# Kernel tuning notes

Measured on AMD Instinct MI355X. Metric: run time of the kernel, lower is better.

## Reference

```python
import jax, jax.numpy as jnp
import numpy as np
from jax import lax


def ternarize(w):
    # TWN-style ternarization: threshold delta = 0.7*mean|w|, scale alpha =
    # mean |w| over surviving entries; straight-through in backward.
    aw = jnp.abs(w)
    delta = 0.7 * jnp.mean(aw)
    mask = (aw > delta).astype(w.dtype)
    alpha = jnp.sum(aw * mask) / jnp.maximum(jnp.sum(mask), 1.0)
    q = alpha * jnp.sign(w) * mask
    return w + lax.stop_gradient(q - w)


def conv2d(x, w, b):
    # x: [N,C,H,W], w: [O,I,kh,kw]
    y = lax.conv_general_dilated(x, w, window_strides=(1, 1), padding='VALID',
                                 dimension_numbers=('NCHW', 'OIHW', 'NCHW'))
    return y + b[None, :, None, None]


def maxpool2(x):
    return lax.reduce_window(x, -jnp.inf, lax.max,
                             window_dimensions=(1, 1, 2, 2),
                             window_strides=(1, 1, 2, 2), padding='VALID')


def setup_inputs() -> dict:
    key = jax.random.key(0)
    ks = jax.random.split(key, 11)
    n_classes = 10
    x = jax.random.normal(ks[0], (1024, 1, 32, 32), dtype=jnp.float32)
    # Kaiming-ish scaled params
    w1 = jax.random.normal(ks[1], (32, 1, 5, 5), jnp.float32) * (1.0 / np.sqrt(1 * 25))
    b1 = jnp.zeros((32,), jnp.float32)
    w2 = jax.random.normal(ks[2], (64, 32, 5, 5), jnp.float32) * (1.0 / np.sqrt(32 * 25))
    b2 = jnp.zeros((64,), jnp.float32)
    w3 = jax.random.normal(ks[3], (120, 64, 5, 5), jnp.float32) * (1.0 / np.sqrt(64 * 25))
    b3 = jnp.zeros((120,), jnp.float32)
    fw1 = jax.random.normal(ks[4], (84, 120), jnp.float32) * (1.0 / np.sqrt(120))
    fb1 = jnp.zeros((84,), jnp.float32)
    fw2 = jax.random.normal(ks[5], (n_classes, 84), jnp.float32) * (1.0 / np.sqrt(84))
    fb2 = jnp.zeros((n_classes,), jnp.float32)
    return {"x": x, "w1": w1, "b1": b1, "w2": w2, "b2": b2,
            "w3": w3, "b3": b3, "fw1": fw1, "fb1": fb1, "fw2": fw2, "fb2": fb2}


def reference(x, w1, b1, w2, b2, w3, b3, fw1, fb1, fw2, fb2):
    h = jnp.tanh(conv2d(x, ternarize(w1), b1))   # [N,32,28,28]
    h = maxpool2(h)                              # [N,32,14,14]
    h = jnp.tanh(conv2d(h, ternarize(w2), b2))   # [N,64,10,10]
    h = maxpool2(h)                              # [N,64,5,5]
    h = jnp.tanh(conv2d(h, ternarize(w3), b3))   # [N,120,1,1]
    h = h.reshape(h.shape[0], -1)                # [N,120]
    h = jnp.tanh(h @ ternarize(fw1).T + fb1)     # [N,84]
    logits = h @ ternarize(fw2).T + fb2          # [N,n_classes]
    probs = jax.nn.softmax(logits, axis=1)
    return (logits, probs)
```

## Files before the change

kernel.cpp:

```cpp
#include <hip/hip_runtime.h>
#include <hip/hip_bf16.h>
#include <math.h>


typedef __attribute__((ext_vector_type(8))) short bf16x8;
typedef __attribute__((ext_vector_type(4))) float f32x4;

static const size_t OFF_PB    = 0;
static const size_t OFF_W1B   = 256;
static const size_t OFF_W2B   = 1056;
static const size_t OFF_W3B   = 26656;
static const size_t OFF_FW1T  = 129056;
static const size_t OFF_FW2T  = 139136;
static const size_t OFF_P2B   = 139976;
static const size_t OFF_H3    = 959176;

#define BPT 16

__device__ __forceinline__ ushort f2bf(float v) {
    unsigned u = __float_as_uint(v);
    unsigned r = (u + 0x7FFFu + ((u >> 16) & 1u)) >> 16;
    return (ushort)r;
}
__device__ __forceinline__ float bf2f(ushort h) {
    return __uint_as_float((unsigned)h << 16);
}

__device__ __forceinline__ float tanh_fast(float x) {
    float e = __expf(-2.0f * fabsf(x));
    float r = 1.0f - 2.0f * e / (1.0f + e);
    return copysignf(r, x);
}

__device__ __forceinline__ void tensor_select(int tensor,
        const float* w1, const float* w2, const float* w3,
        const float* fw1, const float* fw2,
        const float*& src, int& O, int& K) {
    switch (tensor) {
        case 0: src = w1;  O = 32;  K = 25;   break;
        case 1: src = w2;  O = 64;  K = 800;  break;
        case 2: src = w3;  O = 120; K = 1600; break;
        case 3: src = fw1; O = 84;  K = 120;  break;
        default: src = fw2; O = 10; K = 84;   break;
    }
}

__device__ __forceinline__ float block_sum_256(float v, float* sbuf) {
    #pragma unroll
    for (int off = 32; off > 0; off >>= 1) v += __shfl_down(v, off);
    const int wid = threadIdx.x >> 6;
    if ((threadIdx.x & 63) == 0) sbuf[wid] = v;
    __syncthreads();
    return sbuf[0] + sbuf[1] + sbuf[2] + sbuf[3];
}

__device__ __forceinline__ float alpha_of(const float* pb, int tensor) {
    float s1 = 0.f, c = 0.f;
    #pragma unroll
    for (int i = 0; i < BPT; ++i) {
        s1 += pb[80 + tensor * BPT + i];
        c  += pb[160 + tensor * BPT + i];
    }
    return s1 / fmaxf(c, 1.0f);
}

__global__ __launch_bounds__(256)
void tern_pass1(const float* w1, const float* w2, const float* w3,
                const float* fw1, const float* fw2, float* pb) {
    __shared__ float sbuf[4];
    const int tensor = blockIdx.x / BPT;
    const int blk    = blockIdx.x % BPT;
    const float* src; int O, K;
    tensor_select(tensor, w1, w2, w3, fw1, fw2, src, O, K);
    const int n = O * K;
    float s = 0.f;
    for (int i = blk * 256 + threadIdx.x; i < n; i += BPT * 256)
        s += fabsf(src[i]);
    s = block_sum_256(s, sbuf);
    if (threadIdx.x == 0) pb[tensor * BPT + blk] = s;
}

__global__ __launch_bounds__(256)
void tern_pass2(const float* w1, const float* w2, const float* w3,
                const float* fw1, const float* fw2,
                ushort* w1b, ushort* w2b, ushort* w3b,
                float* fw1t, float* fw2t, float* pb) {
    __shared__ float sbuf[4];
    const int tensor = blockIdx.x / BPT;
    const int blk    = blockIdx.x % BPT;
    const float* src; int O, K;
    tensor_select(tensor, w1, w2, w3, fw1, fw2, src, O, K);
    const int n = O * K;
    float tot = 0.f;
    #pragma unroll
    for (int i = 0; i < BPT; ++i) tot += pb[tensor * BPT + i];
    const float delta = 0.7f * tot / (float)n;

    const ushort BP = 0x3F80u, BN = 0xBF80u;
    float s1 = 0.f, cnt = 0.f;

    if (tensor == 0) {
        for (int j = blk * 256 + threadIdx.x; j < 1024; j += BPT * 256) {
            const int oc = j >> 5, kk = j & 31;
            ushort qb = 0;
            if (kk < 25) {
                float w = src[oc * 25 + kk];
                float aw = fabsf(w);
                if (aw > delta) { s1 += aw; cnt += 1.f; qb = (w > 0.f) ? BP : BN; }
            }
            w1b[j] = qb;
        }
    } else if (tensor == 2) {
        for (int i = blk * 256 + threadIdx.x; i < 128 * 1600; i += BPT * 256) {
            ushort qb = 0;
            if (i < n) {
                float w = src[i];
                float aw = fabsf(w);
                if (aw > delta) { s1 += aw; cnt += 1.f; qb = (w > 0.f) ? BP : BN; }
            }
            w3b[i] = qb;
        }
    } else if (tensor == 1) {
        for (int i = blk * 256 + threadIdx.x; i < n; i += BPT * 256) {
            float w = src[i];
            float aw = fabsf(w);
            ushort qb = 0;
            if (aw > delta) { s1 += aw; cnt += 1.f; qb = (w > 0.f) ? BP : BN; }
            int oc = i / 800;
            int r  = i - oc * 800;
            int ic = r / 25;
            int tap = r - ic * 25;
            w2b[oc * 800 + tap * 32 + ic] = qb;
        }
    } else {
        float* dst = (tensor == 3) ? fw1t : fw2t;
        for (int i = blk * 256 + threadIdx.x; i < n; i += BPT * 256) {
            float w = src[i];
            float aw = fabsf(w);
            float q = 0.f;
            if (aw > delta) { s1 += aw; cnt += 1.f; q = (w > 0.f) ? 1.f : -1.f; }
            int o = i / K;
            int k = i - o * K;
            dst[k * O + o] = q;
        }
    }
    s1 = block_sum_256(s1, sbuf);
    __syncthreads();
    cnt = block_sum_256(cnt, sbuf);
    if (threadIdx.x == 0) {
        pb[80 + tensor * BPT + blk]  = s1;
        pb[160 + tensor * BPT + blk] = cnt;
    }
}

#define C2PF 4
__device__ __forceinline__ void conv2_all(
        const ushort* __restrict__ w2b, const ushort* sxt,
        int n0, int mt0, int lane, f32x4 acc[4][2]) {
    const int col = lane & 15, quad = lane >> 4;
    const ushort* abase[4];
    #pragma unroll
    for (int mi = 0; mi < 4; ++mi) {
        int m = (mt0 + mi) * 16 + col;
        m = m < 100 ? m : 99;
        const int oh = m / 10, ow = m - oh * 10;
        abase[mi] = sxt + (oh * 14 + ow) * 40 + quad * 8;
    }
    const ushort* wb0 = w2b + (size_t)(n0 + col) * 800 + quad * 8;
    const ushort* wb1 = wb0 + 16 * 800;
    bf16x8 pb0[C2PF], pb1[C2PF];
    #pragma unroll
    for (int i = 0; i < C2PF; ++i) {
        pb0[i] = *(const bf16x8*)(wb0 + i * 32);
        pb1[i] = *(const bf16x8*)(wb1 + i * 32);
    }
    #pragma unroll
    for (int tap = 0; tap < 25; ++tap) {
        const int slot = tap & (C2PF - 1);
        const bf16x8 b0 = pb0[slot];
        const bf16x8 b1 = pb1[slot];
        if (tap + C2PF < 25) {
            pb0[slot] = *(const bf16x8*)(wb0 + (tap + C2PF) * 32);
            pb1[slot] = *(const bf16x8*)(wb1 + (tap + C2PF) * 32);
        }
        const int kh = tap / 5, kw = tap - kh * 5;
        const int aoff = (kh * 14 + kw) * 40;
        #pragma unroll
        for (int mi = 0; mi < 4; ++mi) {
            bf16x8 af = *(const bf16x8*)(abase[mi] + aoff);
            acc[mi][0] = __builtin_amdgcn_mfma_f32_16x16x32_bf16(af, b0, acc[mi][0], 0, 0, 0);
            acc[mi][1] = __builtin_amdgcn_mfma_f32_16x16x32_bf16(af, b1, acc[mi][1], 0, 0, 0);
        }
    }
}

__global__ __launch_bounds__(256, 4)
void conv12_kernel(const float* __restrict__ x, const ushort* __restrict__ w1b,
                   const float* __restrict__ b1, const ushort* __restrict__ w2b,
                   const float* __restrict__ b2, const float* __restrict__ pb,
                   ushort* __restrict__ p2b) {
    __shared__ __align__(16) char smem[40776];
    ushort* A      = (ushort*)smem;
    ushort* sxt    = (ushort*)smem;
    ushort* hb1    = (ushort*)(smem + 15680);
    float*  hb2    = (float*) (smem + 15680);
    ushort* sxb    = (ushort*)(smem + 38720);
    float*  salpha = (float*) (smem + 40768);

    const int n = blockIdx.x;
    const int t = threadIdx.x;
    const int wave = t >> 6, lane = t & 63;
    const int col = lane & 15, quad = lane >> 4;

    bf16x8 B0 = *(const bf16x8*)(w1b + col * 32 + quad * 8);
    bf16x8 B1 = *(const bf16x8*)(w1b + (col + 16) * 32 + quad * 8);

    {
        float4 v = ((const float4*)(x + (size_t)n * 1024))[t];
        ushort4 q;
        q.x = f2bf(v.x); q.y = f2bf(v.y); q.z = f2bf(v.z); q.w = f2bf(v.w);
        *(ushort4*)(sxb + t * 4) = q;
        if (t == 0) salpha[0] = alpha_of(pb, 0);
        if (t == 1) salpha[1] = alpha_of(pb, 1);
    }
    __syncthreads();

    #pragma unroll
    for (int c = 0; c < 4; ++c) {
        const int tbase = c * 13;
        const int ct    = (c == 3) ? 10 : 13;
        const int pbase = tbase * 16;
        const int rows  = ct * 16;

        for (int r = t; r < rows; r += 256) {
            const int p = pbase + r;
            const int oh = p / 28, ow = p % 28;
            ushort v[25];
            #pragma unroll
            for (int kh = 0; kh < 5; ++kh) {
                const ushort* rr = sxb + (oh + kh) * 32 + ow;
                v[kh*5+0]=rr[0]; v[kh*5+1]=rr[1]; v[kh*5+2]=rr[2];
                v[kh*5+3]=rr[3]; v[kh*5+4]=rr[4];
            }
            uint2* arow = (uint2*)(A + r * 36);
            #pragma unroll
            for (int j = 0; j < 6; ++j) {
                uint2 w;
                w.x = (unsigned)v[4*j]   | ((unsigned)v[4*j+1] << 16);
                w.y = (unsigned)v[4*j+2] | ((unsigned)v[4*j+3] << 16);
                arow[j] = w;
            }
            uint2 w6; w6.x = (unsigned)v[24]; w6.y = 0u;
            arow[6] = w6;
            uint2 w7; w7.x = 0u; w7.y = 0u;
            arow[7] = w7;
        }
        __syncthreads();

        for (int tl = wave; tl < ct; tl += 4) {
            const ushort* ap = A + (tl * 16 + col) * 36 + quad * 8;
            ushort4 lo = *(const ushort4*)ap;
            ushort4 hi = *(const ushort4*)(ap + 4);
            bf16x8 af;
            af[0]=(short)lo.x; af[1]=(short)lo.y; af[2]=(short)lo.z; af[3]=(short)lo.w;
            af[4]=(short)hi.x; af[5]=(short)hi.y; af[6]=(short)hi.z; af[7]=(short)hi.w;
            f32x4 z = {};
            f32x4 c0 = __builtin_amdgcn_mfma_f32_16x16x32_bf16(af, B0, z, 0, 0, 0);
            f32x4 c1 = __builtin_amdgcn_mfma_f32_16x16x32_bf16(af, B1, z, 0, 0, 0);
            const int p = pbase + tl * 16 + quad * 4;
            const int oh = p / 28, ow2 = (p % 28) >> 1;
            const int pos = oh * 14 + ow2;
            hb1[pos * 32 + col]            = f2bf(fmaxf(c0[0], c0[1]));
            hb1[(pos + 1) * 32 + col]      = f2bf(fmaxf(c0[2], c0[3]));
            hb1[pos * 32 + col + 16]       = f2bf(fmaxf(c1[0], c1[1]));
            hb1[(pos + 1) * 32 + col + 16] = f2bf(fmaxf(c1[2], c1[3]));
        }
        __syncthreads();
    }

    {
        const float a1 = salpha[0];
        const int oc2 = (t & 15) * 2;
        const float b1a = b1[oc2], b1b = b1[oc2 + 1];
        for (int idx = t; idx < 3136; idx += 256) {
            const int pos2 = idx >> 4;
            const int ph = pos2 / 14, pw = pos2 - ph * 14;
            const int in0 = (2 * ph) * 14 + pw;
            const uint u0 = *(const uint*)(hb1 + in0 * 32 + oc2);
            const uint u1 = *(const uint*)(hb1 + (in0 + 14) * 32 + oc2);
            const float m0 = fmaxf(bf2f((ushort)u0), bf2f((ushort)u1));
            const float m1 = fmaxf(bf2f((ushort)(u0 >> 16)), bf2f((ushort)(u1 >> 16)));
            const ushort r0 = f2bf(tanh_fast(fmaf(a1, m0, b1a)));
            const ushort r1 = f2bf(tanh_fast(fmaf(a1, m1, b1b)));
            *(uint*)(sxt + pos2 * 40 + oc2) = (uint)r0 | ((uint)r1 << 16);
        }
    }
    __syncthreads();

    const int n0  = (wave & 1) * 32;
    const int mt0 = (wave >> 1) * 4;
    f32x4 acc2[4][2] = {};
    conv2_all(w2b, sxt, n0, mt0, lane, acc2);

    {
        #pragma unroll
        for (int mi = 0; mi < 4; ++mi) {
            const int mrow = (mt0 + mi) * 16 + quad * 4;
            if (mrow < 100) {
                #pragma unroll
                for (int np = 0; np < 2; ++np) {
                    const int oc = n0 + np * 16 + col;
                    float2 hm;
                    hm.x = fmaxf(acc2[mi][np][0], acc2[mi][np][1]);
                    hm.y = fmaxf(acc2[mi][np][2], acc2[mi][np][3]);
                    *(float2*)(&hb2[oc * 50 + (mrow >> 1)]) = hm;
                }
            }
        }
    }
    __syncthreads();

    const float a2 = salpha[1];
    for (int idx = t; idx < 1600; idx += 256) {
        const int oc = idx / 25, r = idx - oc * 25;
        const int ph = r / 5, pw = r - ph * 5;
        const float* hb = &hb2[oc * 50 + ph * 10 + pw];
        float m = fmaxf(hb[0], hb[5]);
        p2b[(size_t)n * 1600 + idx] = f2bf(tanh_fast(fmaf(a2, m, b2[oc])));
    }
}

template<int STEPS>
__device__ __forceinline__ void conv3_chunk(const ushort* Abase, const ushort* B0,
                                            f32x4& acc0) {
    #pragma unroll
    for (int s = 0; s < STEPS; ++s) {
        bf16x8 af = *(const bf16x8*)(Abase + s * 32);
        bf16x8 b0 = *(const bf16x8*)(B0 + s * 32);
        acc0 = __builtin_amdgcn_mfma_f32_16x16x32_bf16(af, b0, acc0, 0, 0, 0);
    }
}

__global__ __launch_bounds__(256)
void conv3_mfma(const ushort* __restrict__ p2b, const ushort* __restrict__ w3b,
                const float* __restrict__ b3, const float* __restrict__ pb,
                float* __restrict__ h3) {
    __shared__ float red[4][64][4];
    __shared__ float salpha;
    const int t = threadIdx.x;
    const int wave = t >> 6, lane = t & 63;
    const int mt   = blockIdx.x >> 3;
    const int noct = blockIdx.x & 7;
    const int col = lane & 15, quad = lane >> 4;
    const int kstart = (wave < 2) ? wave * 13 : 26 + (wave - 2) * 12;

    if (t == 0) salpha = alpha_of(pb, 2);

    const ushort* Abase = p2b + (size_t)(mt * 16 + col) * 1600 + kstart * 32 + quad * 8;
    const ushort* B0 = w3b + (size_t)(noct * 16 + col) * 1600 + kstart * 32 + quad * 8;

    f32x4 acc0 = {};
    if (wave < 2) conv3_chunk<13>(Abase, B0, acc0);
    else          conv3_chunk<12>(Abase, B0, acc0);

    #pragma unroll
    for (int r = 0; r < 4; ++r) red[wave][lane][r] = acc0[r];
    __syncthreads();

    {
        const float a3 = salpha;
        const int l = t & 63, vh = t >> 6;
        const int lcol = l & 15, lquad = l >> 4;
        const int img = mt * 16 + lquad * 4 + vh;
        float s = red[0][l][vh] + red[1][l][vh] + red[2][l][vh] + red[3][l][vh];
        const int oc = noct * 16 + lcol;
        if (oc < 120) h3[(size_t)img * 120 + oc] = tanh_fast(fmaf(a3, s, b3[oc]));
    }
}

__global__ __launch_bounds__(128)
void fc_kernel(const float* __restrict__ h3, const float* __restrict__ fw1t,
               const float* __restrict__ fb1, const float* __restrict__ fw2t,
               const float* __restrict__ fb2, const float* __restrict__ pb,
               float* __restrict__ out) {
    const int n = blockIdx.x;
    __shared__ float sh[120];
    __shared__ float sh4[84];
    __shared__ float sl[10];
    __shared__ float salpha[2];
    __shared__ __align__(16) float wbuf[2][30 * 84];
    __shared__ __align__(16) float fw2s[84 * 10];
    const int t = threadIdx.x;
    if (t < 120) sh[t] = h3[(size_t)n * 120 + t];
    if (t == 120) salpha[0] = alpha_of(pb, 3);
    if (t == 121) salpha[1] = alpha_of(pb, 4);
    #pragma unroll
    for (int i = 0; i < 2; ++i) {
        const int j = t + i * 128;
        if (j < 210) ((float4*)fw2s)[j] = ((const float4*)fw2t)[j];
    }
    for (int i = t; i < 630; i += 128)
        ((float4*)wbuf[0])[i] = ((const float4*)fw1t)[i];
    __syncthreads();

    float a = 0.f;
    #pragma unroll
    for (int c = 0; c < 4; ++c) {
        if (c < 3) {
            const float4* src = (const float4*)(fw1t + (c + 1) * 2520);
            float4* dst = (float4*)wbuf[(c + 1) & 1];
            for (int i = t; i < 630; i += 128) dst[i] = src[i];
        }
        if (t < 84) {
            const float* wc = wbuf[c & 1];
            #pragma unroll 6
            for (int kk = 0; kk < 30; ++kk)
                a = fmaf(wc[kk * 84 + t], sh[30 * c + kk], a);
        }
        __syncthreads();
    }
    if (t < 84) sh4[t] = tanh_fast(fmaf(salpha[0], a, fb1[t]));
    __syncthreads();
    if (t < 10) {
        const float af2 = salpha[1];
        float a2 = 0.f;
        #pragma unroll 4
        for (int k = 0; k < 84; ++k) a2 = fmaf(fw2s[k * 10 + t], sh4[k], a2);
        const float lg = fmaf(af2, a2, fb2[t]);
        sl[t] = lg;
        out[(size_t)n * 10 + t] = lg;
    }
    __syncthreads();
    if (t < 10) {
        float m = -INFINITY;
        #pragma unroll
        for (int i = 0; i < 10; ++i) m = fmaxf(m, sl[i]);
        float s = 0.f;
        #pragma unroll
        for (int i = 0; i < 10; ++i) s += expf(sl[i] - m);
        out[10240 + (size_t)n * 10 + t] = expf(sl[t] - m) / s;
    }
}

extern "C" void kernel_launch(void* const* d_in, const int* in_sizes, int n_in,
                              void* d_out, int out_size, void* d_ws, size_t ws_size,
                              hipStream_t stream) {
    const float* x   = (const float*)d_in[0];
    const float* w1  = (const float*)d_in[1];
    const float* b1  = (const float*)d_in[2];
    const float* w2  = (const float*)d_in[3];
    const float* b2  = (const float*)d_in[4];
    const float* w3  = (const float*)d_in[5];
    const float* b3  = (const float*)d_in[6];
    const float* fw1 = (const float*)d_in[7];
    const float* fb1 = (const float*)d_in[8];
    const float* fw2 = (const float*)d_in[9];
    const float* fb2 = (const float*)d_in[10];

    float* ws = (float*)d_ws;
    float*  pb   = ws + OFF_PB;
    ushort* w1b  = (ushort*)(ws + OFF_W1B);
    ushort* w2b  = (ushort*)(ws + OFF_W2B);
    ushort* w3b  = (ushort*)(ws + OFF_W3B);
    float*  fw1t = ws + OFF_FW1T;
    float*  fw2t = ws + OFF_FW2T;
    ushort* p2b  = (ushort*)(ws + OFF_P2B);
    float*  h3   = ws + OFF_H3;
    float*  out  = (float*)d_out;

    tern_pass1<<<5 * BPT, 256, 0, stream>>>(w1, w2, w3, fw1, fw2, pb);
    tern_pass2<<<5 * BPT, 256, 0, stream>>>(w1, w2, w3, fw1, fw2,
                                            w1b, w2b, w3b, fw1t, fw2t, pb);
    conv12_kernel<<<1024, 256, 0, stream>>>(x, w1b, b1, w2b, b2, pb, p2b);
    conv3_mfma<<<512, 256, 0, stream>>>(p2b, w3b, b3, pb, h3);
    fc_kernel<<<1024, 128, 0, stream>>>(h3, fw1t, fb1, fw2t, fb2, pb, out);
}
```

Baseline: 153.0 us.

## Fuse conv1 full 2x2 maxpool and tanh into MFMA epilogue via pool-ordered rows

Reorders conv1 im2col rows so each group of four consecutive output positions forms one 2x2 pooling window. The MFMA epilogue can then do the whole max-pool, scale, bias and tanh in registers and write directly to the conv2 input buffer. This removes the intermediate hb1 buffer, its separate pooling pass and one barrier, and shrinks shared memory. Chunking changes from 4 chunks of 13 tiles to 3 chunks of 17/16/16 tiles, which cuts one sync and loop iteration.

```diff
diff --git a/kernel.cpp b/kernel.cpp
--- a/kernel.cpp
+++ b/kernel.cpp
@@ -199,13 +199,12 @@
                    const float* __restrict__ b1, const ushort* __restrict__ w2b,
                    const float* __restrict__ b2, const float* __restrict__ pb,
                    ushort* __restrict__ p2b) {
-    __shared__ __align__(16) char smem[40776];
+    __shared__ __align__(16) char smem[37328];
     ushort* A      = (ushort*)smem;
-    ushort* sxt    = (ushort*)smem;
-    ushort* hb1    = (ushort*)(smem + 15680);
-    float*  hb2    = (float*) (smem + 15680);
-    ushort* sxb    = (ushort*)(smem + 38720);
-    float*  salpha = (float*) (smem + 40768);
+    float*  hb2    = (float*) smem;
+    ushort* sxt    = (ushort*)(smem + 19584);
+    ushort* sxb    = (ushort*)(smem + 35264);
+    float*  salpha = (float*) (smem + 37312);
 
     const int n = blockIdx.x;
     const int t = threadIdx.x;
@@ -214,6 +213,8 @@
 
     bf16x8 B0 = *(const bf16x8*)(w1b + col * 32 + quad * 8);
     bf16x8 B1 = *(const bf16x8*)(w1b + (col + 16) * 32 + quad * 8);
+    const float b1a = b1[col];
+    const float b1b = b1[col + 16];
 
     {
         float4 v = ((const float4*)(x + (size_t)n * 1024))[t];
@@ -225,16 +226,18 @@
     }
     __syncthreads();
 
-    #pragma unroll
-    for (int c = 0; c < 4; ++c) {
-        const int tbase = c * 13;
-        const int ct    = (c == 3) ? 10 : 13;
+    const float a1 = salpha[0];
+    for (int c = 0; c < 3; ++c) {
+        const int tbase = (c == 0) ? 0 : (17 + 16 * (c - 1));
+        const int ct    = (c == 0) ? 17 : 16;
         const int pbase = tbase * 16;
         const int rows  = ct * 16;
 
         for (int r = t; r < rows; r += 256) {
-            const int p = pbase + r;
-            const int oh = p / 28, ow = p % 28;
+            const int p   = pbase + r;
+            const int pb4 = p >> 2, sub = p & 3;
+            const int oh = 2 * (pb4 / 14) + (sub >> 1);
+            const int ow = 2 * (pb4 % 14) + (sub & 1);
             ushort v[25];
             #pragma unroll
             for (int kh = 0; kh < 5; ++kh) {
@@ -267,35 +270,18 @@
             f32x4 z = {};
             f32x4 c0 = __builtin_amdgcn_mfma_f32_16x16x32_bf16(af, B0, z, 0, 0, 0);
             f32x4 c1 = __builtin_amdgcn_mfma_f32_16x16x32_bf16(af, B1, z, 0, 0, 0);
-            const int p = pbase + tl * 16 + quad * 4;
-            const int oh = p / 28, ow2 = (p % 28) >> 1;
-            const int pos = oh * 14 + ow2;
-            hb1[pos * 32 + col]            = f2bf(fmaxf(c0[0], c0[1]));
-            hb1[(pos + 1) * 32 + col]      = f2bf(fmaxf(c0[2], c0[3]));
-            hb1[pos * 32 + col + 16]       = f2bf(fmaxf(c1[0], c1[1]));
-            hb1[(pos + 1) * 32 + col + 16] = f2bf(fmaxf(c1[2], c1[3]));
+            const int pos2 = (pbase >> 2) + tl * 4 + quad;
+            const float h01 = bf2f(f2bf(fmaxf(c0[0], c0[1])));
+            const float h23 = bf2f(f2bf(fmaxf(c0[2], c0[3])));
+            sxt[pos2 * 40 + col] =
+                f2bf(tanh_fast(fmaf(a1, fmaxf(h01, h23), b1a)));
+            const float g01 = bf2f(f2bf(fmaxf(c1[0], c1[1])));
+            const float g23 = bf2f(f2bf(fmaxf(c1[2], c1[3])));
+            sxt[pos2 * 40 + col + 16] =
+                f2bf(tanh_fast(fmaf(a1, fmaxf(g01, g23), b1b)));
         }
         __syncthreads();
     }
-
-    {
-        const float a1 = salpha[0];
-        const int oc2 = (t & 15) * 2;
-        const float b1a = b1[oc2], b1b = b1[oc2 + 1];
-        for (int idx = t; idx < 3136; idx += 256) {
-            const int pos2 = idx >> 4;
-            const int ph = pos2 / 14, pw = pos2 - ph * 14;
-            const int in0 = (2 * ph) * 14 + pw;
-            const uint u0 = *(const uint*)(hb1 + in0 * 32 + oc2);
-            const uint u1 = *(const uint*)(hb1 + (in0 + 14) * 32 + oc2);
-            const float m0 = fmaxf(bf2f((ushort)u0), bf2f((ushort)u1));
-            const float m1 = fmaxf(bf2f((ushort)(u0 >> 16)), bf2f((ushort)(u1 >> 16)));
-            const ushort r0 = f2bf(tanh_fast(fmaf(a1, m0, b1a)));
-            const ushort r1 = f2bf(tanh_fast(fmaf(a1, m1, b1b)));
-            *(uint*)(sxt + pos2 * 40 + oc2) = (uint)r0 | ((uint)r1 << 16);
-        }
-    }
-    __syncthreads();
 
     const int n0  = (wave & 1) * 32;
     const int mt0 = (wave >> 1) * 4;
```

After: 148.9 us. 1.03x faster.
